# Kernel optimization log

Measured on AMD Instinct MI355X. Metric: run time of the kernel, lower is better.

Reference implementation:

```python
import jax, jax.numpy as jnp
import numpy as np

# The 8 structuring elements from the torch module, in order.
_KERNELS = np.array([
    [[1.,1.,1.],[1.,1.,1.],[1.,1.,1.]],
    [[0.,1.,1.],[0.,1.,1.],[0.,1.,1.]],
    [[1.,1.,1.],[1.,1.,1.],[0.,0.,0.]],
    [[0.,0.,0.],[0.,1.,1.],[0.,1.,1.]],
    [[0.,1.,0.],[0.,1.,0.],[0.,1.,0.]],
    [[0.,0.,0.],[1.,1.,1.],[0.,0.,0.]],
    [[0.,1.,0.],[0.,1.,0.],[0.,0.,0.]],
    [[0.,0.,0.],[1.,1.,0.],[0.,0.,0.]],
], dtype=np.float32)


def _conv3x3(x, k):
    # x: [N,1,H,W], k: [3,3] -> same-padded single-channel conv (cross-correlation, like torch conv2d)
    return jax.lax.conv_general_dilated(
        x, k[None, None, :, :], window_strides=(1, 1),
        padding=((1, 1), (1, 1)),
        dimension_numbers=('NCHW', 'OIHW', 'NCHW'))


def setup_inputs() -> dict:
    key = jax.random.key(0)
    N, H, W = 16, 1024, 1024
    x = (jax.random.uniform(key, (N, 1, H, W)) < 0.5).astype(jnp.float32)
    kernels = jnp.asarray(_KERNELS)  # [8,3,3]
    return {"x": x, "kernels": kernels}


def reference(x, kernels):
    output = jnp.zeros_like(x)
    # Sequential loop over the 8 fixed structuring elements (data dependency on x).
    for i in range(8):
        k = kernels[i]
        eroded = _conv3x3(x, k)
        ksum = jnp.sum(k)
        mask = (eroded >= ksum).astype(x.dtype)
        output = jnp.maximum(output, mask)
        # mark(): dilate the mask with the flipped binarized kernel
        dil_k = jnp.flip((k > 0).astype(x.dtype), axis=(0, 1))
        visited = (_conv3x3(mask, dil_k) > 0).astype(x.dtype)
        x = x - visited
    # return_single_point=True branch
    sp = _conv3x3(output, kernels[0])
    output = jnp.where((sp > 0) & (sp < 2), jnp.ones_like(sp), jnp.zeros_like(sp))
    return output
```

## Files before the change

kernel.cpp:

```cpp
#include <hip/hip_runtime.h>
#include <stdint.h>


typedef unsigned long long u64;
typedef float vfloat4 __attribute__((ext_vector_type(4)));

#define WIDTH   1024
#define HEIGHT  1024
#define NIMG    16
#define WPR     16
#define TH      32
#define HALO    16
#define RRROWS  64
#define PR      66
#define PW      18
#define NTHR    512
#define PACK_ROWS 4

__global__ __launch_bounds__(256) void pack_kernel(const float* __restrict__ x,
                                                   u64* __restrict__ packed) {
    int wv = threadIdx.x >> 6, lane = threadIdx.x & 63;
    int row = blockIdx.x * PACK_ROWS + wv;
    const float* rbase = x + (size_t)row * WIDTH;
    u64* pbase = packed + (size_t)row * WPR;
    #pragma unroll
    for (int rnd = 0; rnd < 4; ++rnd) {
        vfloat4 v = *(const vfloat4*)(rbase + rnd * 256 + lane * 4);
        unsigned nib = (v.x > 0.5f ? 1u : 0u) | (v.y > 0.5f ? 2u : 0u)
                     | (v.z > 0.5f ? 4u : 0u) | (v.w > 0.5f ? 8u : 0u);
        u64 n = (u64)nib << (4 * (lane & 15));
        n |= __shfl_xor(n, 1);
        n |= __shfl_xor(n, 2);
        n |= __shfl_xor(n, 4);
        n |= __shfl_xor(n, 8);
        if ((lane & 15) == 0) pbase[rnd * 4 + (lane >> 4)] = n;
    }
}

template <int CM>
__device__ __forceinline__ u64 hand(const u64* Ar, int w) {
    u64 c = Ar[w], res = ~0ULL;
    if (CM & 2) res &= c;
    if (CM & 1) res &= (c << 1) | (Ar[w - 1] >> 63);
    if (CM & 4) res &= (c >> 1) | (Ar[w + 1] << 63);
    return res;
}
template <int CM>
__device__ __forceinline__ u64 hor(const u64* Ar, int w) {
    u64 c = Ar[w], res = 0;
    if (CM & 2) res |= c;
    if (CM & 1) res |= (c >> 1) | (Ar[w + 1] << 63);
    if (CM & 4) res |= (c << 1) | (Ar[w - 1] >> 63);
    return res;
}
template <int RM>
__device__ __forceinline__ u64 vand(const u64 (*A)[PW], int r, int w) {
    u64 res = ~0ULL;
    if (RM & 1) res &= A[r - 1][w];
    if (RM & 2) res &= A[r][w];
    if (RM & 4) res &= A[r + 1][w];
    return res;
}
template <int RM>
__device__ __forceinline__ u64 vor(const u64 (*A)[PW], int r, int w) {
    u64 res = 0;
    if (RM & 1) res |= A[r + 1][w];
    if (RM & 2) res |= A[r][w];
    if (RM & 4) res |= A[r - 1][w];
    return res;
}

template <int R, typename F>
__device__ __forceinline__ void forcells(F f) {
    for (int idx = threadIdx.x; idx < (TH + 2 * R) * WPR; idx += NTHR) {
        int r = 17 - R + (idx >> 4);
        int w = 1 + (idx & 15);
        f(r, w);
    }
    __syncthreads();
}

template <int RM, int CM, int HR, int MR, int DHR, int BR, bool DIL>
__device__ __forceinline__ void morph_step(u64 (&B)[PR][PW], u64 (&T)[PR][PW],
                                           u64 (&M)[PR][PW], u64 (&O)[PR][PW]) {
    if (CM != 2 && RM != 2) {
        forcells<HR>([&](int r, int w) { T[r][w] = hand<CM>(B[r], w); });
        forcells<MR>([&](int r, int w) {
            u64 m = vand<RM>(T, r, w); M[r][w] = m; O[r][w] |= m;
        });
    } else if (CM == 2) {
        forcells<MR>([&](int r, int w) {
            u64 m = vand<RM>(B, r, w); M[r][w] = m; O[r][w] |= m;
        });
    } else {
        forcells<MR>([&](int r, int w) {
            u64 m = hand<CM>(B[r], w); M[r][w] = m; O[r][w] |= m;
        });
    }
    if (DIL) {
        if (CM != 2 && RM != 2) {
            forcells<DHR>([&](int r, int w) { T[r][w] = hor<CM>(M[r], w); });
            forcells<BR>([&](int r, int w) { B[r][w] &= ~vor<RM>(T, r, w); });
        } else if (CM == 2) {
            forcells<BR>([&](int r, int w) { B[r][w] &= ~vor<RM>(M, r, w); });
        } else {
            forcells<BR>([&](int r, int w) { B[r][w] &= ~hor<CM>(M[r], w); });
        }
    }
}

__global__ __launch_bounds__(NTHR) void morph_kernel(const u64* __restrict__ packed,
                                                     float* __restrict__ out) {
    __shared__ u64 B[PR][PW];
    __shared__ u64 T[PR][PW];
    __shared__ u64 M[PR][PW];
    __shared__ u64 O[PR][PW];
    int tid = threadIdx.x;
    int ty = blockIdx.x, img = blockIdx.y;

    {
        u64* bf = &B[0][0]; u64* mf = &M[0][0]; u64* of = &O[0][0];
        for (int i = tid; i < PR * PW; i += NTHR) { bf[i] = 0; mf[i] = 0; of[i] = 0; }
    }
    __syncthreads();

    const u64* pimg = packed + (size_t)img * HEIGHT * WPR;
    for (int idx = tid; idx < RRROWS * WPR; idx += NTHR) {
        int rr = idx >> 4, w = idx & 15;
        int gy = ty * TH - HALO + rr;
        if (gy >= 0 && gy < HEIGHT)
            B[rr + 1][w + 1] = pimg[(size_t)gy * WPR + w];
    }
    __syncthreads();

    morph_step<7, 7, 16, 15, 15, 14, true >(B, T, M, O);
    morph_step<7, 6, 14, 13, 13, 12, true >(B, T, M, O);
    morph_step<3, 7, 12, 11, 11, 10, true >(B, T, M, O);
    morph_step<6, 6, 10,  9,  9,  8, true >(B, T, M, O);
    morph_step<7, 2,  8,  7,  7,  6, true >(B, T, M, O);
    morph_step<2, 7,  6,  5,  5,  4, true >(B, T, M, O);
    morph_step<3, 2,  4,  3,  3,  2, true >(B, T, M, O);
    morph_step<2, 3,  2,  1,  1,  0, false>(B, T, M, O);

    forcells<0>([&](int r, int w) {
        u64 ones = 0;
        u64 twos = 0;
        #pragma unroll
        for (int dr = -1; dr <= 1; ++dr) {
            const u64* Ar = O[r + dr];
            u64 c  = Ar[w];
            u64 wv = (c << 1) | (Ar[w - 1] >> 63);
            u64 ev = (c >> 1) | (Ar[w + 1] << 63);
            twos |= ones & wv; ones ^= wv;
            twos |= ones & c;  ones ^= c;
            twos |= ones & ev; ones ^= ev;
        }
        T[r][w] = ones & ~twos;
    });

    float* obase = out + ((size_t)img * HEIGHT + (size_t)ty * TH) * WIDTH;
    for (int idx = tid; idx < TH * (WIDTH / 4); idx += NTHR) {
        int row = idx >> 8;
        int q   = idx & 255;
        u64 word = T[17 + row][1 + (q >> 4)];
        int b = (q & 15) * 4;
        vfloat4 v;
        v.x = (float)((word >> (b + 0)) & 1ULL);
        v.y = (float)((word >> (b + 1)) & 1ULL);
        v.z = (float)((word >> (b + 2)) & 1ULL);
        v.w = (float)((word >> (b + 3)) & 1ULL);
        __builtin_nontemporal_store(v, (vfloat4*)(obase + (size_t)row * WIDTH + q * 4));
    }
}

extern "C" void kernel_launch(void* const* d_in, const int* in_sizes, int n_in,
                              void* d_out, int out_size, void* d_ws, size_t ws_size,
                              hipStream_t stream) {
    const float* x = (const float*)d_in[0];
    float* out = (float*)d_out;
    u64* packed = (u64*)d_ws;

    hipLaunchKernelGGL(pack_kernel, dim3(NIMG * HEIGHT / PACK_ROWS), dim3(256), 0,
                       stream, x, packed);
    hipLaunchKernelGGL(morph_kernel, dim3(HEIGHT / TH, NIMG), dim3(NTHR), 0, stream,
                       packed, out);
}
```

Baseline: 117.4 us.

## Move bit-packed morphology into per-wave registers with shuffle-based vertical neighbors

Replaces the shared-memory tiled morphology kernel with one where each wavefront owns a 64-bit column strip and a band of 128 rows (2 rows per lane, with left/right neighbor words in registers). Vertical neighbor access uses cross-lane shuffles instead of LDS reads, which removes the many __syncthreads and shared-memory passes of the original. The cost is redundant halo work: each wave recomputes neighbor words and 17-row halos, so only 94 of 128 rows are valid output. The output is staged through a small shared buffer and written with coalesced float4 stores.

```diff
diff --git a/kernel.cpp b/kernel.cpp
--- a/kernel.cpp
+++ b/kernel.cpp
@@ -9,12 +9,11 @@
 #define HEIGHT  1024
 #define NIMG    16
 #define WPR     16
-#define TH      32
-#define HALO    16
-#define RRROWS  64
-#define PR      66
-#define PW      18
-#define NTHR    512
+#define RPL     2
+#define VROWS   128
+#define HALO    17
+#define BVALID  94
+#define NBANDS  11
 #define PACK_ROWS 4
 
 __global__ __launch_bounds__(256) void pack_kernel(const float* __restrict__ x,
@@ -37,139 +36,152 @@
     }
 }
 
-template <int CM>
-__device__ __forceinline__ u64 hand(const u64* Ar, int w) {
-    u64 c = Ar[w], res = ~0ULL;
-    if (CM & 2) res &= c;
-    if (CM & 1) res &= (c << 1) | (Ar[w - 1] >> 63);
-    if (CM & 4) res &= (c >> 1) | (Ar[w + 1] << 63);
-    return res;
-}
-template <int CM>
-__device__ __forceinline__ u64 hor(const u64* Ar, int w) {
-    u64 c = Ar[w], res = 0;
-    if (CM & 2) res |= c;
-    if (CM & 1) res |= (c >> 1) | (Ar[w + 1] << 63);
-    if (CM & 4) res |= (c << 1) | (Ar[w - 1] >> 63);
-    return res;
-}
-template <int RM>
-__device__ __forceinline__ u64 vand(const u64 (*A)[PW], int r, int w) {
-    u64 res = ~0ULL;
-    if (RM & 1) res &= A[r - 1][w];
-    if (RM & 2) res &= A[r][w];
-    if (RM & 4) res &= A[r + 1][w];
-    return res;
-}
-template <int RM>
-__device__ __forceinline__ u64 vor(const u64 (*A)[PW], int r, int w) {
-    u64 res = 0;
-    if (RM & 1) res |= A[r + 1][w];
-    if (RM & 2) res |= A[r][w];
-    if (RM & 4) res |= A[r - 1][w];
-    return res;
-}
-
-template <int R, typename F>
-__device__ __forceinline__ void forcells(F f) {
-    for (int idx = threadIdx.x; idx < (TH + 2 * R) * WPR; idx += NTHR) {
-        int r = 17 - R + (idx >> 4);
-        int w = 1 + (idx & 15);
-        f(r, w);
+__device__ __forceinline__ u64 sh_up(u64 x, int lane) {
+    u64 t = __shfl(x, lane - 1);
+    return lane == 0 ? 0ULL : t;
+}
+__device__ __forceinline__ u64 sh_dn(u64 x, int lane) {
+    u64 t = __shfl(x, lane + 1);
+    return lane == 63 ? 0ULL : t;
+}
+
+template <int RM, int CM, bool DIL>
+__device__ __forceinline__ void mstep(u64 (&B)[RPL][3], u64 (&O)[RPL][3], int lane) {
+    u64 T[RPL][3], M[RPL][3];
+    #pragma unroll
+    for (int s = 0; s < RPL; ++s) {
+        #pragma unroll
+        for (int j = 0; j < 3; ++j) {
+            u64 c = B[s][j], res = ~0ULL;
+            if (CM & 2) res &= c;
+            if (CM & 1) res &= (c << 1) | ((j > 0 ? B[s][j - 1] : 0ULL) >> 63);
+            if (CM & 4) res &= (c >> 1) | ((j < 2 ? B[s][j + 1] : 0ULL) << 63);
+            T[s][j] = res;
+        }
+    }
+    #pragma unroll
+    for (int j = 0; j < 3; ++j) {
+        u64 up = sh_up(T[RPL - 1][j], lane);
+        u64 dn = sh_dn(T[0][j], lane);
+        #pragma unroll
+        for (int s = 0; s < RPL; ++s) {
+            u64 res = ~0ULL;
+            if (RM & 2) res &= T[s][j];
+            if (RM & 1) res &= (s > 0 ? T[s - 1][j] : up);
+            if (RM & 4) res &= (s < RPL - 1 ? T[s + 1][j] : dn);
+            M[s][j] = res;
+            O[s][j] |= res;
+        }
+    }
+    if (DIL) {
+        #pragma unroll
+        for (int s = 0; s < RPL; ++s) {
+            #pragma unroll
+            for (int j = 0; j < 3; ++j) {
+                u64 c = M[s][j], res = 0;
+                if (CM & 2) res |= c;
+                if (CM & 1) res |= (c >> 1) | ((j < 2 ? M[s][j + 1] : 0ULL) << 63);
+                if (CM & 4) res |= (c << 1) | ((j > 0 ? M[s][j - 1] : 0ULL) >> 63);
+                T[s][j] = res;
+            }
+        }
+        #pragma unroll
+        for (int j = 0; j < 3; ++j) {
+            u64 up = sh_up(T[RPL - 1][j], lane);
+            u64 dn = sh_dn(T[0][j], lane);
+            #pragma unroll
+            for (int s = 0; s < RPL; ++s) {
+                u64 res = 0;
+                if (RM & 2) res |= T[s][j];
+                if (RM & 1) res |= (s < RPL - 1 ? T[s + 1][j] : dn);
+                if (RM & 4) res |= (s > 0 ? T[s - 1][j] : up);
+                B[s][j] &= ~res;
+            }
+        }
+    }
+}
+
+__global__ __launch_bounds__(256) void regmorph_kernel(const u64* __restrict__ packed,
+                                                       float* __restrict__ out) {
+    __shared__ u64 stage[4][BVALID + 2];
+    int lane = threadIdx.x & 63;
+    int wv = threadIdx.x >> 6;
+    int W = blockIdx.x * 4 + wv;
+    int img  = W / (WPR * NBANDS);
+    int rem  = W % (WPR * NBANDS);
+    int wcol = rem / NBANDS;
+    int band = rem % NBANDS;
+    int bstart = band * BVALID - HALO;
+
+    const u64* pimg = packed + (size_t)img * HEIGHT * WPR;
+    u64 B[RPL][3], O[RPL][3];
+    #pragma unroll
+    for (int s = 0; s < RPL; ++s) {
+        int g = bstart + lane * RPL + s;
+        bool rok = (g >= 0 && g < HEIGHT);
+        #pragma unroll
+        for (int j = 0; j < 3; ++j) {
+            int wi = wcol - 1 + j;
+            B[s][j] = (rok && wi >= 0 && wi < WPR) ? pimg[(size_t)g * WPR + wi] : 0ULL;
+            O[s][j] = 0ULL;
+        }
+    }
+
+    mstep<7, 7, true >(B, O, lane);
+    mstep<7, 6, true >(B, O, lane);
+    mstep<3, 7, true >(B, O, lane);
+    mstep<6, 6, true >(B, O, lane);
+    mstep<7, 2, true >(B, O, lane);
+    mstep<2, 7, true >(B, O, lane);
+    mstep<3, 2, true >(B, O, lane);
+    mstep<2, 3, false>(B, O, lane);
+
+    u64 Wn[RPL], Cn[RPL], En[RPL], res[RPL];
+    #pragma unroll
+    for (int s = 0; s < RPL; ++s) {
+        Cn[s] = O[s][1];
+        Wn[s] = (O[s][1] << 1) | (O[s][0] >> 63);
+        En[s] = (O[s][1] >> 1) | (O[s][2] << 63);
+    }
+    u64 upW = sh_up(Wn[RPL - 1], lane), upC = sh_up(Cn[RPL - 1], lane),
+        upE = sh_up(En[RPL - 1], lane);
+    u64 dnW = sh_dn(Wn[0], lane), dnC = sh_dn(Cn[0], lane), dnE = sh_dn(En[0], lane);
+    #pragma unroll
+    for (int s = 0; s < RPL; ++s) {
+        u64 ones = 0, twos = 0;
+        auto acc = [&](u64 v) { twos |= ones & v; ones ^= v; };
+        acc(s > 0 ? Wn[s - 1] : upW);
+        acc(s > 0 ? Cn[s - 1] : upC);
+        acc(s > 0 ? En[s - 1] : upE);
+        acc(Wn[s]); acc(Cn[s]); acc(En[s]);
+        acc(s < RPL - 1 ? Wn[s + 1] : dnW);
+        acc(s < RPL - 1 ? Cn[s + 1] : dnC);
+        acc(s < RPL - 1 ? En[s + 1] : dnE);
+        res[s] = ones & ~twos;
+    }
+
+    #pragma unroll
+    for (int s = 0; s < RPL; ++s) {
+        int v = lane * RPL + s;
+        if (v >= HALO && v < HALO + BVALID) stage[wv][v - HALO] = res[s];
     }
     __syncthreads();
-}
-
-template <int RM, int CM, int HR, int MR, int DHR, int BR, bool DIL>
-__device__ __forceinline__ void morph_step(u64 (&B)[PR][PW], u64 (&T)[PR][PW],
-                                           u64 (&M)[PR][PW], u64 (&O)[PR][PW]) {
-    if (CM != 2 && RM != 2) {
-        forcells<HR>([&](int r, int w) { T[r][w] = hand<CM>(B[r], w); });
-        forcells<MR>([&](int r, int w) {
-            u64 m = vand<RM>(T, r, w); M[r][w] = m; O[r][w] |= m;
-        });
-    } else if (CM == 2) {
-        forcells<MR>([&](int r, int w) {
-            u64 m = vand<RM>(B, r, w); M[r][w] = m; O[r][w] |= m;
-        });
-    } else {
-        forcells<MR>([&](int r, int w) {
-            u64 m = hand<CM>(B[r], w); M[r][w] = m; O[r][w] |= m;
-        });
-    }
-    if (DIL) {
-        if (CM != 2 && RM != 2) {
-            forcells<DHR>([&](int r, int w) { T[r][w] = hor<CM>(M[r], w); });
-            forcells<BR>([&](int r, int w) { B[r][w] &= ~vor<RM>(T, r, w); });
-        } else if (CM == 2) {
-            forcells<BR>([&](int r, int w) { B[r][w] &= ~vor<RM>(M, r, w); });
-        } else {
-            forcells<BR>([&](int r, int w) { B[r][w] &= ~hor<CM>(M[r], w); });
-        }
-    }
-}
-
-__global__ __launch_bounds__(NTHR) void morph_kernel(const u64* __restrict__ packed,
-                                                     float* __restrict__ out) {
-    __shared__ u64 B[PR][PW];
-    __shared__ u64 T[PR][PW];
-    __shared__ u64 M[PR][PW];
-    __shared__ u64 O[PR][PW];
-    int tid = threadIdx.x;
-    int ty = blockIdx.x, img = blockIdx.y;
-
-    {
-        u64* bf = &B[0][0]; u64* mf = &M[0][0]; u64* of = &O[0][0];
-        for (int i = tid; i < PR * PW; i += NTHR) { bf[i] = 0; mf[i] = 0; of[i] = 0; }
-    }
-    __syncthreads();
-
-    const u64* pimg = packed + (size_t)img * HEIGHT * WPR;
-    for (int idx = tid; idx < RRROWS * WPR; idx += NTHR) {
-        int rr = idx >> 4, w = idx & 15;
-        int gy = ty * TH - HALO + rr;
-        if (gy >= 0 && gy < HEIGHT)
-            B[rr + 1][w + 1] = pimg[(size_t)gy * WPR + w];
-    }
-    __syncthreads();
-
-    morph_step<7, 7, 16, 15, 15, 14, true >(B, T, M, O);
-    morph_step<7, 6, 14, 13, 13, 12, true >(B, T, M, O);
-    morph_step<3, 7, 12, 11, 11, 10, true >(B, T, M, O);
-    morph_step<6, 6, 10,  9,  9,  8, true >(B, T, M, O);
-    morph_step<7, 2,  8,  7,  7,  6, true >(B, T, M, O);
-    morph_step<2, 7,  6,  5,  5,  4, true >(B, T, M, O);
-    morph_step<3, 2,  4,  3,  3,  2, true >(B, T, M, O);
-    morph_step<2, 3,  2,  1,  1,  0, false>(B, T, M, O);
-
-    forcells<0>([&](int r, int w) {
-        u64 ones = 0;
-        u64 twos = 0;
-        #pragma unroll
-        for (int dr = -1; dr <= 1; ++dr) {
-            const u64* Ar = O[r + dr];
-            u64 c  = Ar[w];
-            u64 wv = (c << 1) | (Ar[w - 1] >> 63);
-            u64 ev = (c >> 1) | (Ar[w + 1] << 63);
-            twos |= ones & wv; ones ^= wv;
-            twos |= ones & c;  ones ^= c;
-            twos |= ones & ev; ones ^= ev;
-        }
-        T[r][w] = ones & ~twos;
-    });
-
-    float* obase = out + ((size_t)img * HEIGHT + (size_t)ty * TH) * WIDTH;
-    for (int idx = tid; idx < TH * (WIDTH / 4); idx += NTHR) {
-        int row = idx >> 8;
-        int q   = idx & 255;
-        u64 word = T[17 + row][1 + (q >> 4)];
-        int b = (q & 15) * 4;
-        vfloat4 v;
-        v.x = (float)((word >> (b + 0)) & 1ULL);
-        v.y = (float)((word >> (b + 1)) & 1ULL);
-        v.z = (float)((word >> (b + 2)) & 1ULL);
-        v.w = (float)((word >> (b + 3)) & 1ULL);
-        __builtin_nontemporal_store(v, (vfloat4*)(obase + (size_t)row * WIDTH + q * 4));
+
+    int gbase = band * BVALID;
+    float* obase = out + (size_t)img * HEIGHT * WIDTH + wcol * 64 + (lane & 15) * 4;
+    for (int it = 0; it < (BVALID + 3) / 4; ++it) {
+        int t = it * 4 + (lane >> 4);
+        int g = gbase + t;
+        if (t < BVALID && g < HEIGHT) {
+            u64 word = stage[wv][t];
+            unsigned nib = (unsigned)(word >> ((lane & 15) * 4)) & 15u;
+            vfloat4 v4;
+            v4.x = (nib & 1) ? 1.f : 0.f;
+            v4.y = (nib & 2) ? 1.f : 0.f;
+            v4.z = (nib & 4) ? 1.f : 0.f;
+            v4.w = (nib & 8) ? 1.f : 0.f;
+            __builtin_nontemporal_store(v4, (vfloat4*)(obase + (size_t)g * WIDTH));
+        }
     }
 }
 
@@ -182,6 +194,7 @@
 
     hipLaunchKernelGGL(pack_kernel, dim3(NIMG * HEIGHT / PACK_ROWS), dim3(256), 0,
                        stream, x, packed);
-    hipLaunchKernelGGL(morph_kernel, dim3(HEIGHT / TH, NIMG), dim3(NTHR), 0, stream,
+    hipLaunchKernelGGL(regmorph_kernel,
+                       dim3(NIMG * WPR * NBANDS / 4), dim3(256), 0, stream,
                        packed, out);
 }
```

After: 116.6 us. About the same (-0.6%).
